# Kernel optimization log

Hardware: AMD Instinct MI355X
Metric: run time of the kernel (lower is better)

The kernel has to match this reference:

```python
import jax, jax.numpy as jnp
import numpy as np

KH, KW, PAD = 3, 3, 1
K = KH * KW


def _offset_conv(x, w, b):
    # standard 3x3 conv, stride 1, padding 1, NCHW
    out = jax.lax.conv_general_dilated(
        x, w, window_strides=(1, 1), padding=((PAD, PAD), (PAD, PAD)),
        dimension_numbers=("NCHW", "OIHW", "NCHW"))
    return out + b[None, :, None, None]


def _deform_conv(x, offsets, weight, groups):
    # torchvision.ops.deform_conv2d semantics: offset channels are
    # (dy, dx) pairs per kernel tap; zero padding outside the image;
    # bilinear interpolation with per-corner validity masks.
    B, C, H, W = x.shape
    off = offsets.reshape(B, K, 2, H, W)
    dy, dx = off[:, :, 0], off[:, :, 1]                      # [B,K,H,W]

    ky, kx = jnp.meshgrid(jnp.arange(KH), jnp.arange(KW), indexing="ij")
    ky = ky.reshape(K); kx = kx.reshape(K)
    base_y = (jnp.arange(H)[None, :, None] + (ky - PAD)[:, None, None])  # [K,H,1]
    base_x = (jnp.arange(W)[None, None, :] + (kx - PAD)[:, None, None])  # [K,1,W]
    py = base_y[None].astype(x.dtype) + dy                   # [B,K,H,W]
    px = base_x[None].astype(x.dtype) + dx

    # torchvision returns 0 when the sample point is fully outside
    valid = (py > -1) & (py < H) & (px > -1) & (px < W)
    y0 = jnp.floor(py); x0 = jnp.floor(px)
    ly = py - y0; lx = px - x0                               # fractional parts
    y0i = y0.astype(jnp.int32); x0i = x0.astype(jnp.int32)

    def gather(yi, xi):
        ok = (yi >= 0) & (yi < H) & (xi >= 0) & (xi < W) & valid
        yic = jnp.clip(yi, 0, H - 1)
        xic = jnp.clip(xi, 0, W - 1)
        def per_b(img, yb, xb, okb):
            # img [C,H,W]; yb,xb,okb [K,H,W] -> [C,K,H,W]
            return img[:, yb, xb] * okb[None].astype(img.dtype)
        return jax.vmap(per_b)(x, yic, xic, ok)

    v00 = gather(y0i, x0i)
    v01 = gather(y0i, x0i + 1)
    v10 = gather(y0i + 1, x0i)
    v11 = gather(y0i + 1, x0i + 1)
    w00 = ((1 - ly) * (1 - lx))[:, None]
    w01 = ((1 - ly) * lx)[:, None]
    w10 = (ly * (1 - lx))[:, None]
    w11 = (ly * lx)[:, None]
    sampled = v00 * w00 + v01 * w01 + v10 * w10 + v11 * w11  # [B,C,K,H,W]

    Cg = C // groups
    sampled = sampled.reshape(B, groups, Cg, K, H, W)
    wg = weight.reshape(groups, Cg, Cg, K)                   # [G, Cout_g, Cin_g, K]
    out = jnp.einsum("bgckhw,gock->bgohw", sampled, wg)
    return out.reshape(B, C, H, W)


def setup_inputs() -> dict:
    key = jax.random.key(0)
    k1, k2, k3, k4 = jax.random.split(key, 4)
    B, C, H, W, groups = 4, 256, 96, 96, 4
    x = jax.random.normal(k1, (B, C, H, W), dtype=jnp.float32)
    # small offset-conv weights keep learned offsets in a realistic range
    offset_w = jax.random.normal(k2, (2 * K, C, KH, KW), dtype=jnp.float32) * 0.02
    offset_b = jax.random.normal(k3, (2 * K,), dtype=jnp.float32) * 0.1
    fan_in = (C // groups) * KH * KW
    weight = jax.random.normal(k4, (C, C // groups, KH, KW), dtype=jnp.float32) / np.sqrt(fan_in)
    return {"x": x, "offset_w": offset_w, "offset_b": offset_b,
            "weight": weight, "groups": groups}


def reference(x, offset_w, offset_b, weight, groups):
    offsets = _offset_conv(x, offset_w, offset_b)
    return _deform_conv(x, offsets, weight, groups)
```

## Files before the change

### kernel.cpp

```cpp
#include <hip/hip_runtime.h>
#include <hip/hip_bf16.h>
#include <math.h>

#define B_   4
#define C_   256
#define H_   96
#define W_   96
#define HW_  (H_ * W_)
#define G_   4
#define CG_  64
#define K_   9
#define PW_  98
#define PROW_ (PW_ * C_)

typedef __bf16  bf16x8 __attribute__((ext_vector_type(8)));
typedef float   f32x4  __attribute__((ext_vector_type(4)));

__global__ __launch_bounds__(256) void prep_kernel(
    const float* __restrict__ ow, const float* __restrict__ wt,
    __hip_bfloat16* __restrict__ aOW, __hip_bfloat16* __restrict__ aW)
{
    int idx = blockIdx.x * 256 + threadIdx.x;
    if (idx < 73728) {
        int j    = idx & 7;
        int r    = idx >> 3;
        int lane = r & 63;  r >>= 6;
        int mt   = r & 1;   r >>= 1;
        int ks   = r & 7;   r >>= 3;
        int tap  = r;
        int m = mt * 16 + (lane & 15);
        int c = ks * 32 + (lane >> 4) * 8 + j;
        float v = (m < 18) ? ow[(m * 256 + c) * 9 + tap] : 0.f;
        aOW[idx] = __float2bfloat16(v);
    }
    if (idx < 147456) {
        int j    = idx & 7;
        int r    = idx >> 3;
        int lane = r & 63;  r >>= 6;
        int ct   = r & 1;   r >>= 1;
        int half = r & 1;   r >>= 1;
        int ks   = r & 1;   r >>= 1;
        int tap  = r % 9;
        int g    = r / 9;
        int c  = ks * 32 + (lane >> 4) * 8 + j;
        int co = half * 32 + ct * 16 + (lane & 15);
        float v = wt[(((g * CG_ + co) * CG_ + c) * 9) + tap];
        aW[idx] = __float2bfloat16(v);
    }
}

__global__ __launch_bounds__(256) void transpose_kernel(
    const float* __restrict__ x, __hip_bfloat16* __restrict__ xtp)
{
    int blk = blockIdx.x;
    int b = blk / H_, h = blk - b * H_;
    int t = threadIdx.x;
    __shared__ __align__(16) __hip_bfloat16 tile[96 * 264];
    const float* xb = x + (size_t)b * C_ * HW_ + h * W_;
    for (int r = 0; r < 96; ++r) {
        int e = r * 256 + t;
        int c = e / 96, w = e - c * 96;
        tile[w * 264 + c] = __float2bfloat16(xb[c * HW_ + w]);
    }
    __syncthreads();
    __hip_bfloat16* ob = xtp + ((size_t)(b * PW_ + h + 1) * PW_ + 1) * C_;
#pragma unroll
    for (int i = 0; i < 12; ++i) {
        int sIdx = i * 256 + t;
        int px = sIdx >> 5, seg = sIdx & 31;
        *(bf16x8*)(ob + px * 256 + seg * 8) =
            *(const bf16x8*)(&tile[px * 264 + seg * 8]);
    }
    bf16x8 z = {};
    if (t < 64) {
        int side = t >> 5, i = t & 31;
        *(bf16x8*)(xtp + ((size_t)(b * PW_ + h + 1) * PW_ + side * 97) * C_ + i * 8) = z;
    }
    if (h == 0 || h == 95) {
        int row = (h == 0) ? 0 : 97;
        __hip_bfloat16* rb = xtp + (size_t)(b * PW_ + row) * PROW_;
#pragma unroll
        for (int i = 0; i < 13; ++i) {
            int idx = i * 256 + t;
            if (idx < 3136) *(bf16x8*)(rb + idx * 8) = z;
        }
    }
}

__global__ __launch_bounds__(768) void offset_conv_kernel(
    const __hip_bfloat16* __restrict__ xtp, const __hip_bfloat16* __restrict__ aOW,
    const float* __restrict__ bias, __hip_bfloat16* __restrict__ off2)
{
    int blk = blockIdx.x;
    int xcd = blk & 7;
    int s   = blk >> 3;
    int bh  = xcd * 48 + s;
    int b   = bh / H_, h = bh % H_;
    int t = threadIdx.x, lane = t & 63;
    int ww = __builtin_amdgcn_readfirstlane(t >> 6);
    int nt = ww % 6;
    int kh = ww / 6;
    int w0 = nt * 16;
    int ml = lane & 15, kq = lane >> 4;

    __shared__ __align__(16) __hip_bfloat16 aS[2][8192];
    __shared__ __align__(16) f32x4 red[6 * 64 * 2];

    auto stage = [&](int tap, int p) {
        const bf16x8* src = (const bf16x8*)(aOW + tap * 8192);
        bf16x8* dst = (bf16x8*)aS[p];
        for (int i = t; i < 1024; i += 768) dst[i] = src[i];
    };

    f32x4 acc0 = {}, acc1 = {};
    const __hip_bfloat16* xb = xtp + (size_t)b * (PW_ * PROW_);

    stage(0, 0);
    __syncthreads();
    for (int tap = 0; tap < 9; ++tap) {
        if (tap < 8) stage(tap + 1, (tap + 1) & 1);
        int ky = tap / 3, kx = tap - ky * 3;
        const __hip_bfloat16* brow =
            xb + ((h + ky) * PW_ + (w0 + ml + kx)) * C_ + kh * 128 + kq * 8;
        const __hip_bfloat16* arow = aS[tap & 1] + kh * 4096 + lane * 8;
#pragma unroll
        for (int ks = 0; ks < 4; ++ks) {
            bf16x8 bf = *(const bf16x8*)(brow + ks * 32);
            bf16x8 a0 = *(const bf16x8*)(arow + ks * 1024);
            bf16x8 a1 = *(const bf16x8*)(arow + ks * 1024 + 512);
            acc0 = __builtin_amdgcn_mfma_f32_16x16x32_bf16(a0, bf, acc0, 0, 0, 0);
            acc1 = __builtin_amdgcn_mfma_f32_16x16x32_bf16(a1, bf, acc1, 0, 0, 0);
        }
        __syncthreads();
    }

    if (kh == 1) {
        red[(nt * 64 + lane) * 2 + 0] = acc0;
        red[(nt * 64 + lane) * 2 + 1] = acc1;
    }
    __syncthreads();
    if (kh == 0) {
        acc0 += red[(nt * 64 + lane) * 2 + 0];
        acc1 += red[(nt * 64 + lane) * 2 + 1];
        int w = w0 + ml;
#pragma unroll
        for (int r = 0; r < 4; ++r) {
            int j0 = kq * 4 + r;
            off2[((size_t)(b * 9 + (j0 >> 1)) * HW_ + h * W_ + w) * 2 + (j0 & 1)] =
                __float2bfloat16(acc0[r] + bias[j0]);
            int j1 = 16 + kq * 4 + r;
            if (j1 < 18)
                off2[((size_t)(b * 9 + (j1 >> 1)) * HW_ + h * W_ + w) * 2 + (j1 & 1)] =
                    __float2bfloat16(acc1[r] + bias[j1]);
        }
    }
}

__global__ __launch_bounds__(384, 4) void deform_kernel(
    const __hip_bfloat16* __restrict__ xtp, const __hip_bfloat16* __restrict__ off2,
    const __hip_bfloat16* __restrict__ aW, float* __restrict__ out)
{
    int blk = blockIdx.x;
    int xcd = blk & 7;
    int s   = blk >> 3;
    int bg  = xcd * 2 + (s / H_);
    int h   = s % H_;
    int g   = bg & 3;
    int b   = bg >> 2;
    int t    = threadIdx.x;
    int lane = t & 63;
    int wave = __builtin_amdgcn_readfirstlane(t >> 6);
    int half   = wave & 1;
    int wthird = wave >> 1;

    __shared__ __align__(16) __hip_bfloat16 sS[2][96 * 72];

    const __hip_bfloat16* xb =
        xtp + ((size_t)b * (PW_ * PW_) + PW_ + 1) * C_ + g * CG_;
    const __hip_bfloat162* offp =
        (const __hip_bfloat162*)off2 + (size_t)(b * 9) * HW_ + h * W_;
    const __hip_bfloat16* aWg = aW + (g * 9) * 4096;

    int tw8 = t >> 3;
    int j8  = (t & 7) * 8;

    f32x4 acc[2][2] = {};

    auto sample = [&](int k, int p) {
        int ky = k / 3, kx = k - ky * 3;
#pragma unroll
        for (int it = 0; it < 2; ++it) {
            int w  = it * 48 + tw8;
            __hip_bfloat162 pr = offp[k * HW_ + w];
            float py = (float)(h + ky - 1) + __bfloat162float(pr.x);
            float px = (float)(w + kx - 1) + __bfloat162float(pr.y);
            bool valid = (py > -1.f) && (py < (float)H_) &&
                         (px > -1.f) && (px < (float)W_);
            float y0f = floorf(py), x0f = floorf(px);
            float ly = py - y0f, lx = px - x0f;
            int y0 = (int)y0f, x0 = (int)x0f;
            int base = valid ? (y0 * PW_ + x0) * C_ : -(PW_ + 1) * C_;
            float wy1 = valid ? ly : 0.f;
            float wy0 = valid ? (1.f - ly) : 0.f;
            float mx0 = 1.f - lx;
            float bw00 = wy0 * mx0, bw01 = wy0 * lx;
            float bw10 = wy1 * mx0, bw11 = wy1 * lx;
            const __hip_bfloat16* p0 = xb + base + j8;
            bf16x8 c00 = *(const bf16x8*)(p0);
            bf16x8 c01 = *(const bf16x8*)(p0 + C_);
            bf16x8 c10 = *(const bf16x8*)(p0 + PROW_);
            bf16x8 c11 = *(const bf16x8*)(p0 + PROW_ + C_);
            bf16x8 r;
#pragma unroll
            for (int e = 0; e < 8; ++e) {
                float v = bw00 * (float)c00[e] + bw01 * (float)c01[e]
                        + bw10 * (float)c10[e] + bw11 * (float)c11[e];
                r[e] = (__bf16)v;
            }
            *(bf16x8*)(&sS[p][w * 72 + j8]) = r;
        }
    };

    auto mmtap = [&](int k, int p) {
        bf16x8 afrag[2][2];
        const __hip_bfloat16* at = aWg + k * 4096 + half * 1024 + lane * 8;
#pragma unroll
        for (int ks = 0; ks < 2; ++ks)
#pragma unroll
            for (int ct = 0; ct < 2; ++ct)
                afrag[ks][ct] = *(const bf16x8*)(at + ks * 2048 + ct * 512);
#pragma unroll
        for (int ks = 0; ks < 2; ++ks) {
#pragma unroll
            for (int wt = 0; wt < 2; ++wt) {
                int wrow = wthird * 32 + wt * 16 + (lane & 15);
                bf16x8 bfrag = *(const bf16x8*)(
                    &sS[p][wrow * 72 + ks * 32 + (lane >> 4) * 8]);
                acc[0][wt] = __builtin_amdgcn_mfma_f32_16x16x32_bf16(
                                 afrag[ks][0], bfrag, acc[0][wt], 0, 0, 0);
                acc[1][wt] = __builtin_amdgcn_mfma_f32_16x16x32_bf16(
                                 afrag[ks][1], bfrag, acc[1][wt], 0, 0, 0);
            }
        }
    };

    sample(0, 0);
    __syncthreads();
    for (int k = 0; k < K_; ++k) {
        if (k < K_ - 1) sample(k + 1, (k + 1) & 1);
        mmtap(k, k & 1);
        __syncthreads();
    }

    float* ob = out + ((b * C_ + g * CG_ + half * 32) * HW_) + h * W_ + wthird * 32;
    int rbase = (lane >> 4) * 4;
    int ncol  = lane & 15;
#pragma unroll
    for (int ct = 0; ct < 2; ++ct)
#pragma unroll
        for (int wt = 0; wt < 2; ++wt)
#pragma unroll
            for (int r = 0; r < 4; ++r)
                __builtin_nontemporal_store(
                    acc[ct][wt][r],
                    ob + (ct * 16 + rbase + r) * HW_ + wt * 16 + ncol);
}

extern "C" void kernel_launch(void* const* d_in, const int* in_sizes, int n_in,
                              void* d_out, int out_size, void* d_ws, size_t ws_size,
                              hipStream_t stream) {
    const float* x    = (const float*)d_in[0];
    const float* ow   = (const float*)d_in[1];
    const float* obi  = (const float*)d_in[2];
    const float* wt   = (const float*)d_in[3];

    __hip_bfloat16* xtp  = (__hip_bfloat16*)d_ws;
    __hip_bfloat16* off2 = xtp + (size_t)B_ * PW_ * PW_ * C_;
    __hip_bfloat16* aW   = off2 + (size_t)B_ * 9 * HW_ * 2;
    __hip_bfloat16* aOW  = aW + 147456;

    prep_kernel<<<576, 256, 0, stream>>>(ow, wt, aOW, aW);
    transpose_kernel<<<B_ * H_, 256, 0, stream>>>(x, xtp);
    offset_conv_kernel<<<B_ * H_, 768, 0, stream>>>(xtp, aOW, obi, off2);
    deform_kernel<<<B_ * G_ * H_, 384, 0, stream>>>(xtp, off2, aW, (float*)d_out);
}
```

Baseline: 177.2 us.

## Split transpose/offset-conv grids and software-pipeline deform gather with MFMA

The transpose and offset-conv kernels now split each (b,h) unit into two halves, by channel and by width respectively. This doubles the grid and shrinks per-block LDS and thread counts. The deform kernel splits sampling into offset load, corner gather and blend stages, so the global gathers for tap k+1 are in flight while the MFMAs for tap k run. It also raises the occupancy hint to 6 waves-blocks per CU. The cost is more live registers, which may not fit the tighter launch bound, plus some redundant staging of offset weights across twice as many blocks.

```diff
diff --git a/kernel.cpp b/kernel.cpp
--- a/kernel.cpp
+++ b/kernel.cpp
@@ -53,63 +53,67 @@
     const float* __restrict__ x, __hip_bfloat16* __restrict__ xtp)
 {
     int blk = blockIdx.x;
-    int b = blk / H_, h = blk - b * H_;
+    int ch  = blk & 1;
+    int bh  = blk >> 1;
+    int b = bh / H_, h = bh - b * H_;
     int t = threadIdx.x;
-    __shared__ __align__(16) __hip_bfloat16 tile[96 * 264];
-    const float* xb = x + (size_t)b * C_ * HW_ + h * W_;
-    for (int r = 0; r < 96; ++r) {
+    __shared__ __align__(16) __hip_bfloat16 tile[96 * 136];
+    const float* xb = x + (size_t)b * C_ * HW_ + (size_t)(ch * 128) * HW_ + h * W_;
+    for (int r = 0; r < 48; ++r) {
         int e = r * 256 + t;
         int c = e / 96, w = e - c * 96;
-        tile[w * 264 + c] = __float2bfloat16(xb[c * HW_ + w]);
+        tile[w * 136 + c] = __float2bfloat16(xb[c * HW_ + w]);
     }
     __syncthreads();
-    __hip_bfloat16* ob = xtp + ((size_t)(b * PW_ + h + 1) * PW_ + 1) * C_;
-#pragma unroll
-    for (int i = 0; i < 12; ++i) {
+    __hip_bfloat16* ob = xtp + ((size_t)(b * PW_ + h + 1) * PW_ + 1) * C_ + ch * 128;
+#pragma unroll
+    for (int i = 0; i < 6; ++i) {
         int sIdx = i * 256 + t;
-        int px = sIdx >> 5, seg = sIdx & 31;
+        int px = sIdx >> 4, seg = sIdx & 15;
         *(bf16x8*)(ob + px * 256 + seg * 8) =
-            *(const bf16x8*)(&tile[px * 264 + seg * 8]);
+            *(const bf16x8*)(&tile[px * 136 + seg * 8]);
     }
     bf16x8 z = {};
-    if (t < 64) {
-        int side = t >> 5, i = t & 31;
-        *(bf16x8*)(xtp + ((size_t)(b * PW_ + h + 1) * PW_ + side * 97) * C_ + i * 8) = z;
+    if (t < 32) {
+        int side = t >> 4, i = t & 15;
+        *(bf16x8*)(xtp + ((size_t)(b * PW_ + h + 1) * PW_ + side * 97) * C_
+                   + ch * 128 + i * 8) = z;
     }
     if (h == 0 || h == 95) {
         int row = (h == 0) ? 0 : 97;
         __hip_bfloat16* rb = xtp + (size_t)(b * PW_ + row) * PROW_;
-#pragma unroll
-        for (int i = 0; i < 13; ++i) {
+        for (int i = 0; i < 7; ++i) {
             int idx = i * 256 + t;
-            if (idx < 3136) *(bf16x8*)(rb + idx * 8) = z;
-        }
-    }
-}
-
-__global__ __launch_bounds__(768) void offset_conv_kernel(
+            if (idx < 1568) *(bf16x8*)(rb + (ch * 1568 + idx) * 8) = z;
+        }
+    }
+}
+
+__global__ __launch_bounds__(384) void offset_conv_kernel(
     const __hip_bfloat16* __restrict__ xtp, const __hip_bfloat16* __restrict__ aOW,
     const float* __restrict__ bias, __hip_bfloat16* __restrict__ off2)
 {
     int blk = blockIdx.x;
     int xcd = blk & 7;
     int s   = blk >> 3;
-    int bh  = xcd * 48 + s;
+    int unit = xcd * 96 + s;
+    int bh   = unit >> 1;
+    int whalf = unit & 1;
     int b   = bh / H_, h = bh % H_;
     int t = threadIdx.x, lane = t & 63;
     int ww = __builtin_amdgcn_readfirstlane(t >> 6);
-    int nt = ww % 6;
-    int kh = ww / 6;
-    int w0 = nt * 16;
+    int nt = ww % 3;
+    int kh = ww / 3;
+    int w0 = whalf * 48 + nt * 16;
     int ml = lane & 15, kq = lane >> 4;
 
     __shared__ __align__(16) __hip_bfloat16 aS[2][8192];
-    __shared__ __align__(16) f32x4 red[6 * 64 * 2];
+    __shared__ __align__(16) f32x4 red[3 * 64 * 2];
 
     auto stage = [&](int tap, int p) {
         const bf16x8* src = (const bf16x8*)(aOW + tap * 8192);
         bf16x8* dst = (bf16x8*)aS[p];
-        for (int i = t; i < 1024; i += 768) dst[i] = src[i];
+        for (int i = t; i < 1024; i += 384) dst[i] = src[i];
     };
 
     f32x4 acc0 = {}, acc1 = {};
@@ -156,7 +160,7 @@
     }
 }
 
-__global__ __launch_bounds__(384, 4) void deform_kernel(
+__global__ __launch_bounds__(384, 6) void deform_kernel(
     const __hip_bfloat16* __restrict__ xtp, const __hip_bfloat16* __restrict__ off2,
     const __hip_bfloat16* __restrict__ aW, float* __restrict__ out)
 {
@@ -186,14 +190,23 @@
 
     f32x4 acc[2][2] = {};
 
-    auto sample = [&](int k, int p) {
+    __hip_bfloat162 pr[2];
+    bf16x8 c00[2], c01[2], c10[2], c11[2];
+    float bw00[2], bw01[2], bw10[2], bw11[2];
+
+    auto ld_off = [&](int k) {
+#pragma unroll
+        for (int it = 0; it < 2; ++it)
+            pr[it] = offp[k * HW_ + it * 48 + tw8];
+    };
+
+    auto gather = [&](int k) {
         int ky = k / 3, kx = k - ky * 3;
 #pragma unroll
         for (int it = 0; it < 2; ++it) {
             int w  = it * 48 + tw8;
-            __hip_bfloat162 pr = offp[k * HW_ + w];
-            float py = (float)(h + ky - 1) + __bfloat162float(pr.x);
-            float px = (float)(w + kx - 1) + __bfloat162float(pr.y);
+            float py = (float)(h + ky - 1) + __bfloat162float(pr[it].x);
+            float px = (float)(w + kx - 1) + __bfloat162float(pr[it].y);
             bool valid = (py > -1.f) && (py < (float)H_) &&
                          (px > -1.f) && (px < (float)W_);
             float y0f = floorf(py), x0f = floorf(px);
@@ -203,18 +216,25 @@
             float wy1 = valid ? ly : 0.f;
             float wy0 = valid ? (1.f - ly) : 0.f;
             float mx0 = 1.f - lx;
-            float bw00 = wy0 * mx0, bw01 = wy0 * lx;
-            float bw10 = wy1 * mx0, bw11 = wy1 * lx;
+            bw00[it] = wy0 * mx0; bw01[it] = wy0 * lx;
+            bw10[it] = wy1 * mx0; bw11[it] = wy1 * lx;
             const __hip_bfloat16* p0 = xb + base + j8;
-            bf16x8 c00 = *(const bf16x8*)(p0);
-            bf16x8 c01 = *(const bf16x8*)(p0 + C_);
-            bf16x8 c10 = *(const bf16x8*)(p0 + PROW_);
-            bf16x8 c11 = *(const bf16x8*)(p0 + PROW_ + C_);
+            c00[it] = *(const bf16x8*)(p0);
+            c01[it] = *(const bf16x8*)(p0 + C_);
+            c10[it] = *(const bf16x8*)(p0 + PROW_);
+            c11[it] = *(const bf16x8*)(p0 + PROW_ + C_);
+        }
+    };
+
+    auto finish = [&](int p) {
+#pragma unroll
+        for (int it = 0; it < 2; ++it) {
+            int w = it * 48 + tw8;
             bf16x8 r;
 #pragma unroll
             for (int e = 0; e < 8; ++e) {
-                float v = bw00 * (float)c00[e] + bw01 * (float)c01[e]
-                        + bw10 * (float)c10[e] + bw11 * (float)c11[e];
+                float v = bw00[it] * (float)c00[it][e] + bw01[it] * (float)c01[it][e]
+                        + bw10[it] * (float)c10[it][e] + bw11[it] * (float)c11[it][e];
                 r[e] = (__bf16)v;
             }
             *(bf16x8*)(&sS[p][w * 72 + j8]) = r;
@@ -222,34 +242,41 @@
     };
 
     auto mmtap = [&](int k, int p) {
-        bf16x8 afrag[2][2];
         const __hip_bfloat16* at = aWg + k * 4096 + half * 1024 + lane * 8;
 #pragma unroll
-        for (int ks = 0; ks < 2; ++ks)
-#pragma unroll
-            for (int ct = 0; ct < 2; ++ct)
-                afrag[ks][ct] = *(const bf16x8*)(at + ks * 2048 + ct * 512);
-#pragma unroll
         for (int ks = 0; ks < 2; ++ks) {
+            bf16x8 a0 = *(const bf16x8*)(at + ks * 2048);
+            bf16x8 a1 = *(const bf16x8*)(at + ks * 2048 + 512);
 #pragma unroll
             for (int wt = 0; wt < 2; ++wt) {
                 int wrow = wthird * 32 + wt * 16 + (lane & 15);
                 bf16x8 bfrag = *(const bf16x8*)(
                     &sS[p][wrow * 72 + ks * 32 + (lane >> 4) * 8]);
                 acc[0][wt] = __builtin_amdgcn_mfma_f32_16x16x32_bf16(
-                                 afrag[ks][0], bfrag, acc[0][wt], 0, 0, 0);
+                                 a0, bfrag, acc[0][wt], 0, 0, 0);
                 acc[1][wt] = __builtin_amdgcn_mfma_f32_16x16x32_bf16(
-                                 afrag[ks][1], bfrag, acc[1][wt], 0, 0, 0);
+                                 a1, bfrag, acc[1][wt], 0, 0, 0);
             }
         }
     };
 
-    sample(0, 0);
+    ld_off(0);
+    gather(0);
+    ld_off(1);
+    finish(0);
     __syncthreads();
+
+#pragma unroll
     for (int k = 0; k < K_; ++k) {
-        if (k < K_ - 1) sample(k + 1, (k + 1) & 1);
+        if (k < K_ - 1) {
+            gather(k + 1);
+            if (k < K_ - 2) ld_off(k + 2);
+        }
         mmtap(k, k & 1);
-        __syncthreads();
+        if (k < K_ - 1) {
+            finish((k + 1) & 1);
+            __syncthreads();
+        }
     }
 
     float* ob = out + ((b * C_ + g * CG_ + half * 32) * HW_) + h * W_ + wthird * 32;
@@ -280,7 +307,7 @@
     __hip_bfloat16* aOW  = aW + 147456;
 
     prep_kernel<<<576, 256, 0, stream>>>(ow, wt, aOW, aW);
-    transpose_kernel<<<B_ * H_, 256, 0, stream>>>(x, xtp);
-    offset_conv_kernel<<<B_ * H_, 768, 0, stream>>>(xtp, aOW, obi, off2);
+    transpose_kernel<<<B_ * H_ * 2, 256, 0, stream>>>(x, xtp);
+    offset_conv_kernel<<<B_ * H_ * 2, 384, 0, stream>>>(xtp, aOW, obi, off2);
     deform_kernel<<<B_ * G_ * H_, 384, 0, stream>>>(xtp, off2, aW, (float*)d_out);
 }
```

After: 187.9 us. 6.0% more time.

## Fuse weight prep into transpose, split transpose and offset conv across more blocks

Applied to the files above, without the earlier changes.

Merges the weight-packing prep kernel into the input transpose kernel, removing one launch. The transpose now splits channels into two halves per row, doubling the block count, and reads x with float4 loads instead of scalar loads. The offset conv kernel splits each row into two width halves with 384-thread blocks, doubling the grid for better CU occupancy at the cost of reloading the staged weights twice as often.

```diff
diff --git a/kernel.cpp b/kernel.cpp
--- a/kernel.cpp
+++ b/kernel.cpp
@@ -16,14 +16,17 @@
 typedef __bf16  bf16x8 __attribute__((ext_vector_type(8)));
 typedef float   f32x4  __attribute__((ext_vector_type(4)));
 
-__global__ __launch_bounds__(256) void prep_kernel(
-    const float* __restrict__ ow, const float* __restrict__ wt,
+__global__ __launch_bounds__(256) void transpose_prep_kernel(
+    const float* __restrict__ x, const float* __restrict__ ow,
+    const float* __restrict__ wt, __hip_bfloat16* __restrict__ xtp,
     __hip_bfloat16* __restrict__ aOW, __hip_bfloat16* __restrict__ aW)
 {
-    int idx = blockIdx.x * 256 + threadIdx.x;
-    if (idx < 73728) {
-        int j    = idx & 7;
-        int r    = idx >> 3;
+    int t = threadIdx.x;
+    int gid = blockIdx.x * 256 + t;
+
+    if (gid < 73728) {
+        int j    = gid & 7;
+        int r    = gid >> 3;
         int lane = r & 63;  r >>= 6;
         int mt   = r & 1;   r >>= 1;
         int ks   = r & 7;   r >>= 3;
@@ -31,11 +34,11 @@
         int m = mt * 16 + (lane & 15);
         int c = ks * 32 + (lane >> 4) * 8 + j;
         float v = (m < 18) ? ow[(m * 256 + c) * 9 + tap] : 0.f;
-        aOW[idx] = __float2bfloat16(v);
-    }
-    if (idx < 147456) {
-        int j    = idx & 7;
-        int r    = idx >> 3;
+        aOW[gid] = __float2bfloat16(v);
+    }
+    if (gid < 147456) {
+        int j    = gid & 7;
+        int r    = gid >> 3;
         int lane = r & 63;  r >>= 6;
         int ct   = r & 1;   r >>= 1;
         int half = r & 1;   r >>= 1;
@@ -45,71 +48,76 @@
         int c  = ks * 32 + (lane >> 4) * 8 + j;
         int co = half * 32 + ct * 16 + (lane & 15);
         float v = wt[(((g * CG_ + co) * CG_ + c) * 9) + tap];
-        aW[idx] = __float2bfloat16(v);
-    }
-}
-
-__global__ __launch_bounds__(256) void transpose_kernel(
-    const float* __restrict__ x, __hip_bfloat16* __restrict__ xtp)
-{
+        aW[gid] = __float2bfloat16(v);
+    }
+
     int blk = blockIdx.x;
-    int b = blk / H_, h = blk - b * H_;
-    int t = threadIdx.x;
-    __shared__ __align__(16) __hip_bfloat16 tile[96 * 264];
-    const float* xb = x + (size_t)b * C_ * HW_ + h * W_;
-    for (int r = 0; r < 96; ++r) {
-        int e = r * 256 + t;
-        int c = e / 96, w = e - c * 96;
-        tile[w * 264 + c] = __float2bfloat16(xb[c * HW_ + w]);
-    }
-    __syncthreads();
-    __hip_bfloat16* ob = xtp + ((size_t)(b * PW_ + h + 1) * PW_ + 1) * C_;
-#pragma unroll
-    for (int i = 0; i < 12; ++i) {
+    int ch  = blk & 1;
+    int bh  = blk >> 1;
+    int b = bh / H_, h = bh - b * H_;
+    __shared__ __align__(16) __hip_bfloat16 tile[96 * 136];
+    const float* xb = x + (size_t)b * C_ * HW_ + (size_t)(ch * 128) * HW_ + h * W_;
+#pragma unroll
+    for (int r = 0; r < 12; ++r) {
+        int e4 = r * 256 + t;
+        int c = e4 / 24, w4 = e4 - c * 24;
+        float4 v = *(const float4*)(xb + (size_t)c * HW_ + w4 * 4);
+        int base = (w4 * 4) * 136 + c;
+        tile[base      ] = __float2bfloat16(v.x);
+        tile[base + 136] = __float2bfloat16(v.y);
+        tile[base + 272] = __float2bfloat16(v.z);
+        tile[base + 408] = __float2bfloat16(v.w);
+    }
+    __syncthreads();
+    __hip_bfloat16* ob = xtp + ((size_t)(b * PW_ + h + 1) * PW_ + 1) * C_ + ch * 128;
+#pragma unroll
+    for (int i = 0; i < 6; ++i) {
         int sIdx = i * 256 + t;
-        int px = sIdx >> 5, seg = sIdx & 31;
+        int px = sIdx >> 4, seg = sIdx & 15;
         *(bf16x8*)(ob + px * 256 + seg * 8) =
-            *(const bf16x8*)(&tile[px * 264 + seg * 8]);
+            *(const bf16x8*)(&tile[px * 136 + seg * 8]);
     }
     bf16x8 z = {};
-    if (t < 64) {
-        int side = t >> 5, i = t & 31;
-        *(bf16x8*)(xtp + ((size_t)(b * PW_ + h + 1) * PW_ + side * 97) * C_ + i * 8) = z;
+    if (t < 32) {
+        int side = t >> 4, i = t & 15;
+        *(bf16x8*)(xtp + ((size_t)(b * PW_ + h + 1) * PW_ + side * 97) * C_
+                   + ch * 128 + i * 8) = z;
     }
     if (h == 0 || h == 95) {
         int row = (h == 0) ? 0 : 97;
         __hip_bfloat16* rb = xtp + (size_t)(b * PW_ + row) * PROW_;
-#pragma unroll
-        for (int i = 0; i < 13; ++i) {
+        for (int i = 0; i < 7; ++i) {
             int idx = i * 256 + t;
-            if (idx < 3136) *(bf16x8*)(rb + idx * 8) = z;
-        }
-    }
-}
-
-__global__ __launch_bounds__(768) void offset_conv_kernel(
+            if (idx < 1568) *(bf16x8*)(rb + (ch * 1568 + idx) * 8) = z;
+        }
+    }
+}
+
+__global__ __launch_bounds__(384) void offset_conv_kernel(
     const __hip_bfloat16* __restrict__ xtp, const __hip_bfloat16* __restrict__ aOW,
     const float* __restrict__ bias, __hip_bfloat16* __restrict__ off2)
 {
     int blk = blockIdx.x;
     int xcd = blk & 7;
     int s   = blk >> 3;
-    int bh  = xcd * 48 + s;
+    int unit = xcd * 96 + s;
+    int bh   = unit >> 1;
+    int whalf = unit & 1;
     int b   = bh / H_, h = bh % H_;
     int t = threadIdx.x, lane = t & 63;
     int ww = __builtin_amdgcn_readfirstlane(t >> 6);
-    int nt = ww % 6;
-    int kh = ww / 6;
-    int w0 = nt * 16;
+    int nt = ww % 3;
+    int kh = ww / 3;
+    int w0 = whalf * 48 + nt * 16;
     int ml = lane & 15, kq = lane >> 4;
 
     __shared__ __align__(16) __hip_bfloat16 aS[2][8192];
-    __shared__ __align__(16) f32x4 red[6 * 64 * 2];
+    __shared__ __align__(16) f32x4 red[3 * 64 * 2];
 
     auto stage = [&](int tap, int p) {
         const bf16x8* src = (const bf16x8*)(aOW + tap * 8192);
         bf16x8* dst = (bf16x8*)aS[p];
-        for (int i = t; i < 1024; i += 768) dst[i] = src[i];
+        for (int i = t; i < 1024; i += 384) dst[i] = src[i];
     };
 
     f32x4 acc0 = {}, acc1 = {};
@@ -279,8 +287,7 @@
     __hip_bfloat16* aW   = off2 + (size_t)B_ * 9 * HW_ * 2;
     __hip_bfloat16* aOW  = aW + 147456;
 
-    prep_kernel<<<576, 256, 0, stream>>>(ow, wt, aOW, aW);
-    transpose_kernel<<<B_ * H_, 256, 0, stream>>>(x, xtp);
-    offset_conv_kernel<<<B_ * H_, 768, 0, stream>>>(xtp, aOW, obi, off2);
+    transpose_prep_kernel<<<B_ * H_ * 2, 256, 0, stream>>>(x, ow, wt, xtp, aOW, aW);
+    offset_conv_kernel<<<B_ * H_ * 2, 384, 0, stream>>>(xtp, aOW, obi, off2);
     deform_kernel<<<B_ * G_ * H_, 384, 0, stream>>>(xtp, off2, aW, (float*)d_out);
 }
```

Result: faster. 169.4 us (-4.4%).
